# Kernel tuning notes

Hardware: AMD Instinct MI355X
Metric: run time of the kernel (lower is better)

Reference implementation:

```python
import jax, jax.numpy as jnp
import numpy as np

B, S, H, I, E, K = 2, 512, 768, 3072, 8, 1
LB_COEF = 0.01


def _xavier(key, shape, fan_in, fan_out):
    limit = np.sqrt(6.0 / (fan_in + fan_out)).astype(np.float32)
    return jax.random.uniform(key, shape, jnp.float32, -limit, limit)


def setup_inputs() -> dict:
    key = jax.random.key(0)
    k0, k1, k2, k3 = jax.random.split(key, 4)
    return {
        "hidden_states": jax.random.normal(k0, (B, S, H), jnp.float32),
        "gate_w": _xavier(k1, (E, H), H, E),          # nn.Linear(H, E).weight
        "gate_b": jnp.zeros((E,), jnp.float32),
        "w1": _xavier(k2, (E, I, H), H, I),           # per-expert Linear(H, I).weight
        "b1": jnp.zeros((E, I), jnp.float32),
        "w2": _xavier(k3, (E, H, I), I, H),           # per-expert Linear(I, H).weight
        "b2": jnp.zeros((E, H), jnp.float32),
    }


def reference(hidden_states, gate_w, gate_b, w1, b1, w2, b2):
    b, s, h = hidden_states.shape
    x = hidden_states.reshape(-1, h)                      # [T, H]
    gate_logits = x @ gate_w.T + gate_b                   # [T, E]
    top_vals, top_idx = jax.lax.top_k(gate_logits, K)     # [T, K]
    # softmax over the (single) selected logit in fp32 -> all ones, kept for fidelity
    gate_weights = jax.nn.softmax(top_vals.astype(jnp.float32), axis=-1)  # [T, K]

    # load balancing loss (torch.var is unbiased, ddof=1)
    gate_mean = gate_logits.mean(axis=0)                  # [E]
    gate_var = gate_logits.var(axis=0, ddof=1)            # [E]
    lb_loss = LB_COEF * (gate_var / (gate_mean ** 2 + 1e-8)).mean()

    # dense per-expert FFN (exact math; combine picks the routed expert)
    hmid = jnp.einsum('th,eih->tei', x, w1) + b1          # [T, E, I]
    hmid = jax.nn.gelu(hmid, approximate=False)           # torch nn.GELU (erf)
    y = jnp.einsum('tei,ehi->teh', hmid, w2) + b2         # [T, E, H]

    sel = top_idx[:, 0]                                   # [T]
    y_sel = jnp.take_along_axis(y, sel[:, None, None], axis=1)[:, 0]  # [T, H]
    out = y_sel * gate_weights[:, 0:1]                    # weight == 1.0 for k=1
    return out.reshape(b, s, h), lb_loss
```

## Files before the change

kernel.cpp:

```cpp
#include <hip/hip_runtime.h>
#include <hip/hip_bf16.h>
#include <math.h>

#define Hdim 768
#define Idim 3072
#define Tn   1024
#define En   8
#define LD1  72
#define LD2  136

using v4f     = __attribute__((ext_vector_type(4))) float;
using short8  = __attribute__((ext_vector_type(8))) short;
using short4v = __attribute__((ext_vector_type(4))) short;

__device__ inline unsigned short f2bf(float f) {
    unsigned u = __float_as_uint(f);
    u += 0x7fffu + ((u >> 16) & 1u);
    return (unsigned short)(u >> 16);
}
__device__ inline short4v pack4(float4 v) {
    return short4v{ (short)f2bf(v.x), (short)f2bf(v.y), (short)f2bf(v.z), (short)f2bf(v.w) };
}
__device__ __forceinline__ void gl2lds16(const unsigned short* g, unsigned short* l) {
    __builtin_amdgcn_global_load_lds(
        (const __attribute__((address_space(1))) void*)g,
        (__attribute__((address_space(3))) void*)l, 16, 0, 0);
}

__global__ __launch_bounds__(256) void gate_kernel(
    const float* __restrict__ x, const float* __restrict__ gw, const float* __restrict__ gb,
    float* __restrict__ gsum, float* __restrict__ gsumsq,
    int* __restrict__ count, int* __restrict__ sel)
{
    __shared__ float gws[8 * 772];
    __shared__ float lg[8][8];
    int tid = threadIdx.x;
    long t0 = (long)blockIdx.x * 8;
    for (int i = tid; i < 8 * 768; i += 256) gws[(i / 768) * 772 + (i % 768)] = gw[i];
    __syncthreads();

    int tok = tid >> 5, e = (tid >> 2) & 7, qr = tid & 3;
    const float4* xp = (const float4*)(x + (t0 + tok) * Hdim) + qr * 48;
    const float4* gp = (const float4*)(gws + e * 772) + qr * 48;
    float a0 = 0.f, a1 = 0.f;
#pragma unroll 8
    for (int i = 0; i < 48; i += 2) {
        float4 xa = xp[i], ga = gp[i], xc = xp[i + 1], gc = gp[i + 1];
        a0 += xa.x * ga.x + xa.y * ga.y + xa.z * ga.z + xa.w * ga.w;
        a1 += xc.x * gc.x + xc.y * gc.y + xc.z * gc.z + xc.w * gc.w;
    }
    float acc = a0 + a1;
    acc += __shfl_xor(acc, 1);
    acc += __shfl_xor(acc, 2);
    if (qr == 0) lg[tok][e] = acc + gb[e];
    __syncthreads();

    if (tid < 8) {
        float best = lg[tid][0]; int bi = 0;
        for (int j = 1; j < 8; j++) { float v = lg[tid][j]; if (v > best) { best = v; bi = j; } }
        sel[t0 + tid] = bi;
        atomicAdd(&count[bi], 1);
    } else if (tid < 16) {
        int e2 = tid - 8;
        float s = 0.f, ss = 0.f;
        for (int t2 = 0; t2 < 8; t2++) { float v = lg[t2][e2]; s += v; ss += v * v; }
        atomicAdd(&gsum[e2], s);
        atomicAdd(&gsumsq[e2], ss);
    }
}

__global__ void finalize_kernel(const float* __restrict__ gsum, const float* __restrict__ gsumsq,
                                const int* __restrict__ count,
                                int* __restrict__ offsets, int* __restrict__ cursor,
                                float* __restrict__ out_lb)
{
    if (threadIdx.x == 0) {
        float accr = 0.f;
        for (int e = 0; e < 8; e++) {
            float mean = gsum[e] * (1.0f / 1024.0f);
            float var  = (gsumsq[e] - gsum[e] * mean) * (1.0f / 1023.0f);
            accr += var / (mean * mean + 1e-8f);
        }
        out_lb[0] = 0.01f * accr * 0.125f;
        int off = 0;
        for (int e = 0; e < 8; e++) { offsets[e] = off; cursor[e] = off; off += count[e]; }
    }
}

__global__ __launch_bounds__(256) void scatter_kernel(const int* __restrict__ sel,
                                                      int* __restrict__ cursor,
                                                      int* __restrict__ perm)
{
    int t = blockIdx.x * 256 + threadIdx.x;
    if (t < Tn) {
        int e = sel[t];
        int pos = atomicAdd(&cursor[e], 1);
        perm[pos] = t;
    }
}

__global__ __launch_bounds__(256) void gather_x_kernel(const float* __restrict__ x,
                                                       const int* __restrict__ perm,
                                                       unsigned short* __restrict__ xb)
{
    int slot = blockIdx.x * 4 + (threadIdx.x >> 6);
    int lane = threadIdx.x & 63;
    int t = perm[slot];
    const float4* src = (const float4*)(x + (long)t * Hdim);
    unsigned short* dst = xb + (long)slot * Hdim;
#pragma unroll
    for (int i = 0; i < 3; i++) {
        int c = lane + 64 * i;
        *(short4v*)(dst + c * 4) = pack4(src[c]);
    }
}

__global__ __launch_bounds__(256) void init_out_kernel(const float* __restrict__ b2,
                                                       const int* __restrict__ sel,
                                                       float* __restrict__ out)
{
    int t = blockIdx.x;
    int h = blockIdx.y * 256 + threadIdx.x;
    out[(long)t * Hdim + h] = b2[sel[t] * Hdim + h];
}

__global__ __launch_bounds__(256) void gemm1_kernel(
    const unsigned short* __restrict__ xb, const float* __restrict__ w1, const float* __restrict__ b1,
    const int* __restrict__ count, const int* __restrict__ offsets,
    unsigned short* __restrict__ hmid)
{
    int e = blockIdx.z;
    int nloc = count[e];
    int m0 = blockIdx.y << 7;
    if (m0 >= nloc) return;
    int n0 = blockIdx.x << 5;
    int off = offsets[e];

    __shared__ __align__(16) unsigned short As[128 * 64];
    __shared__ __align__(16) unsigned short Bs[32 * LD1];

    int tid = threadIdx.x;
    int lane = tid & 63, wave = tid >> 6;
    int quad = lane >> 4, l16 = lane & 15;
    int wm = wave << 5;

    const unsigned short* aG[4];
    unsigned short* aL[4];
#pragma unroll
    for (int i = 0; i < 4; i++) {
        int p = (wave * 4 + i) * 64 + lane;
        int row = p >> 3;
        int kc = (p & 7) ^ (row & 7);
        int m = m0 + row; int mm = m < nloc ? m : nloc - 1;
        aG[i] = xb + (long)(off + mm) * Hdim + kc * 8;
        aL[i] = (unsigned short*)As + p * 8;
    }
    int kq = tid & 15, rb = tid >> 4;
    const float* bp0 = w1 + ((long)e * Idim + n0 + rb) * Hdim + kq * 4;
    const float* bp1 = bp0 + (long)16 * Hdim;

    v4f acc[2][2];
#pragma unroll
    for (int i = 0; i < 2; i++)
#pragma unroll
        for (int j = 0; j < 2; j++) acc[i][j] = (v4f){0.f, 0.f, 0.f, 0.f};

    float4 nb0 = *(const float4*)bp0;
    float4 nb1 = *(const float4*)bp1;

    for (int kb = 0; kb < Hdim; kb += 64) {
        __syncthreads();
#pragma unroll
        for (int i = 0; i < 4; i++) gl2lds16(aG[i] + kb, aL[i]);
        *(short4v*)(Bs + rb * LD1 + kq * 4)        = pack4(nb0);
        *(short4v*)(Bs + (rb + 16) * LD1 + kq * 4) = pack4(nb1);
        __syncthreads();
        if (kb + 64 < Hdim) {
            nb0 = *(const float4*)(bp0 + kb + 64);
            nb1 = *(const float4*)(bp1 + kb + 64);
        }
#pragma unroll
        for (int s = 0; s < 2; s++) {
            short8 af[2], bf2[2];
#pragma unroll
            for (int i = 0; i < 2; i++) {
                int r = wm + i * 16 + l16;
                af[i] = *(const short8*)(As + r * 64 + (((s * 4 + quad) ^ (r & 7)) * 8));
            }
#pragma unroll
            for (int j = 0; j < 2; j++)
                bf2[j] = *(const short8*)(Bs + (j * 16 + l16) * LD1 + s * 32 + quad * 8);
#pragma unroll
            for (int i = 0; i < 2; i++)
#pragma unroll
                for (int j = 0; j < 2; j++)
                    acc[i][j] = __builtin_amdgcn_mfma_f32_16x16x32_bf16(af[i], bf2[j], acc[i][j], 0, 0, 0);
        }
    }

#pragma unroll
    for (int i = 0; i < 2; i++) {
        int mr = wm + i * 16 + quad * 4;
#pragma unroll
        for (int r = 0; r < 4; r++) {
            int m = m0 + mr + r;
            if (m >= nloc) continue;
            long slot = off + m;
#pragma unroll
            for (int j = 0; j < 2; j++) {
                int n = n0 + j * 16 + l16;
                float v = acc[i][j][r] + b1[e * Idim + n];
                float g = 0.5f * v * (1.0f + erff(v * 0.70710678118654752f));
                hmid[slot * Idim + n] = f2bf(g);
            }
        }
    }
}

__global__ __launch_bounds__(256) void gemm2_kernel(
    const unsigned short* __restrict__ hmid, const float* __restrict__ w2,
    const int* __restrict__ count, const int* __restrict__ offsets,
    const int* __restrict__ perm, float* __restrict__ out)
{
    int e = blockIdx.z;
    int nloc = count[e];
    int m0 = blockIdx.y << 7;
    if (m0 >= nloc) return;
    int bx = blockIdx.x;
    int n0 = (bx % 24) << 5;
    long kbase = (long)(bx / 24) * 768;
    int off = offsets[e];

    __shared__ __align__(16) unsigned short As[128 * 128];
    __shared__ __align__(16) unsigned short Bs[32 * LD2];

    int tid = threadIdx.x;
    int lane = tid & 63, wave = tid >> 6;
    int quad = lane >> 4, l16 = lane & 15;
    int wm = wave << 5;

    const unsigned short* aG[8];
    unsigned short* aL[8];
#pragma unroll
    for (int i = 0; i < 8; i++) {
        int p = (wave * 8 + i) * 64 + lane;
        int row = p >> 4;
        int kc = (p & 15) ^ (row & 15);
        int m = m0 + row; int mm = m < nloc ? m : nloc - 1;
        aG[i] = hmid + (long)(off + mm) * Idim + kbase + kc * 8;
        aL[i] = (unsigned short*)As + p * 8;
    }
    int kq5 = tid & 31, rb8 = tid >> 5;
    const float* bp[4];
#pragma unroll
    for (int s = 0; s < 4; s++)
        bp[s] = w2 + ((long)e * Hdim + n0 + rb8 + 8 * s) * Idim + kbase + kq5 * 4;

    v4f acc[2][2];
#pragma unroll
    for (int i = 0; i < 2; i++)
#pragma unroll
        for (int j = 0; j < 2; j++) acc[i][j] = (v4f){0.f, 0.f, 0.f, 0.f};

    float4 nb[4];
#pragma unroll
    for (int s = 0; s < 4; s++) nb[s] = *(const float4*)bp[s];

    for (int kb = 0; kb < 768; kb += 128) {
        __syncthreads();
#pragma unroll
        for (int i = 0; i < 8; i++) gl2lds16(aG[i] + kb, aL[i]);
#pragma unroll
        for (int s = 0; s < 4; s++)
            *(short4v*)(Bs + (rb8 + 8 * s) * LD2 + kq5 * 4) = pack4(nb[s]);
        __syncthreads();
        if (kb + 128 < 768) {
#pragma unroll
            for (int s = 0; s < 4; s++) nb[s] = *(const float4*)(bp[s] + kb + 128);
        }
#pragma unroll
        for (int s = 0; s < 4; s++) {
            short8 af[2], bf2[2];
#pragma unroll
            for (int i = 0; i < 2; i++) {
                int r = wm + i * 16 + l16;
                af[i] = *(const short8*)(As + r * 128 + (((s * 4 + quad) ^ (r & 15)) * 8));
            }
#pragma unroll
            for (int j = 0; j < 2; j++)
                bf2[j] = *(const short8*)(Bs + (j * 16 + l16) * LD2 + s * 32 + quad * 8);
#pragma unroll
            for (int i = 0; i < 2; i++)
#pragma unroll
                for (int j = 0; j < 2; j++)
                    acc[i][j] = __builtin_amdgcn_mfma_f32_16x16x32_bf16(af[i], bf2[j], acc[i][j], 0, 0, 0);
        }
    }

#pragma unroll
    for (int i = 0; i < 2; i++) {
        int mr = wm + i * 16 + quad * 4;
#pragma unroll
        for (int r = 0; r < 4; r++) {
            int m = m0 + mr + r;
            if (m >= nloc) continue;
            int t = perm[off + m];
#pragma unroll
            for (int j = 0; j < 2; j++) {
                int n = n0 + j * 16 + l16;
                atomicAdd(out + (long)t * Hdim + n, acc[i][j][r]);
            }
        }
    }
}

extern "C" void kernel_launch(void* const* d_in, const int* in_sizes, int n_in,
                              void* d_out, int out_size, void* d_ws, size_t ws_size,
                              hipStream_t stream)
{
    const float* x  = (const float*)d_in[0];
    const float* gw = (const float*)d_in[1];
    const float* gb = (const float*)d_in[2];
    const float* w1 = (const float*)d_in[3];
    const float* b1 = (const float*)d_in[4];
    const float* w2 = (const float*)d_in[5];
    const float* b2 = (const float*)d_in[6];
    float* out = (float*)d_out;

    float* gsum    = (float*)d_ws;
    float* gsumsq  = gsum + 8;
    int*   count   = (int*)d_ws + 16;
    int*   offsets = (int*)d_ws + 24;
    int*   cursor  = (int*)d_ws + 32;
    int*   sel     = (int*)d_ws + 40;
    int*   perm    = (int*)d_ws + 40 + 1024;
    unsigned short* xb   = (unsigned short*)((char*)d_ws + 8704);
    unsigned short* hmid = (unsigned short*)((char*)d_ws + 8704 + (size_t)Tn * Hdim * 2);

    hipMemsetAsync(d_ws, 0, 160, stream);
    gate_kernel<<<128, 256, 0, stream>>>(x, gw, gb, gsum, gsumsq, count, sel);
    finalize_kernel<<<1, 64, 0, stream>>>(gsum, gsumsq, count, offsets, cursor, out + (long)Tn * Hdim);
    scatter_kernel<<<4, 256, 0, stream>>>(sel, cursor, perm);
    gather_x_kernel<<<256, 256, 0, stream>>>(x, perm, xb);
    init_out_kernel<<<dim3(Tn, 3), 256, 0, stream>>>(b2, sel, out);
    gemm1_kernel<<<dim3(96, 2, 8), 256, 0, stream>>>(xb, w1, b1, count, offsets, hmid);
    gemm2_kernel<<<dim3(96, 2, 8), 256, 0, stream>>>(hmid, w2, count, offsets, perm, out);
}
```

Baseline: 240.5 us.

## Enlarge GEMM tiles, fuse finalize+scatter, fold bias into split-K gemm2

Both expert GEMMs move from a 128x32 to a 128x64 output tile with a 2x2 wave layout and K-step 128. Gemm2's split-K changes from 4 slices of 768 to 8 slices of 384. The grid is reordered so that expert index is blockIdx.x, and adjacent blocks work on different experts. Finalize and scatter are merged into one 1024-thread block that uses an LDS cursor. The init_out kernel is replaced by a memset, with b2 added by the first K-slice during the atomic accumulation. The aim is to cut launches and reuse each A tile across more columns, at the cost of more registers, more atomics, and a perm order that is no longer deterministic.

Result: slower. 250.2 us (+4.0%).

```diff
diff --git a/kernel.cpp b/kernel.cpp
--- a/kernel.cpp
+++ b/kernel.cpp
@@ -6,8 +6,7 @@
 #define Idim 3072
 #define Tn   1024
 #define En   8
-#define LD1  72
-#define LD2  136
+#define LDB  136
 
 using v4f     = __attribute__((ext_vector_type(4))) float;
 using short8  = __attribute__((ext_vector_type(8))) short;
@@ -69,12 +68,15 @@
     }
 }
 
-__global__ void finalize_kernel(const float* __restrict__ gsum, const float* __restrict__ gsumsq,
-                                const int* __restrict__ count,
-                                int* __restrict__ offsets, int* __restrict__ cursor,
-                                float* __restrict__ out_lb)
-{
-    if (threadIdx.x == 0) {
+__global__ __launch_bounds__(1024) void finscat_kernel(
+    const float* __restrict__ gsum, const float* __restrict__ gsumsq,
+    const int* __restrict__ count, int* __restrict__ offsets,
+    const int* __restrict__ sel, int* __restrict__ perm,
+    float* __restrict__ out_lb)
+{
+    __shared__ int lcur[8];
+    int tid = threadIdx.x;
+    if (tid == 0) {
         float accr = 0.f;
         for (int e = 0; e < 8; e++) {
             float mean = gsum[e] * (1.0f / 1024.0f);
@@ -83,20 +85,12 @@
         }
         out_lb[0] = 0.01f * accr * 0.125f;
         int off = 0;
-        for (int e = 0; e < 8; e++) { offsets[e] = off; cursor[e] = off; off += count[e]; }
-    }
-}
-
-__global__ __launch_bounds__(256) void scatter_kernel(const int* __restrict__ sel,
-                                                      int* __restrict__ cursor,
-                                                      int* __restrict__ perm)
-{
-    int t = blockIdx.x * 256 + threadIdx.x;
-    if (t < Tn) {
-        int e = sel[t];
-        int pos = atomicAdd(&cursor[e], 1);
-        perm[pos] = t;
-    }
+        for (int e = 0; e < 8; e++) { offsets[e] = off; lcur[e] = off; off += count[e]; }
+    }
+    __syncthreads();
+    int e = sel[tid];
+    int pos = atomicAdd(&lcur[e], 1);
+    perm[pos] = tid;
 }
 
 __global__ __launch_bounds__(256) void gather_x_kernel(const float* __restrict__ x,
@@ -115,83 +109,78 @@
     }
 }
 
-__global__ __launch_bounds__(256) void init_out_kernel(const float* __restrict__ b2,
-                                                       const int* __restrict__ sel,
-                                                       float* __restrict__ out)
-{
-    int t = blockIdx.x;
-    int h = blockIdx.y * 256 + threadIdx.x;
-    out[(long)t * Hdim + h] = b2[sel[t] * Hdim + h];
-}
-
 __global__ __launch_bounds__(256) void gemm1_kernel(
     const unsigned short* __restrict__ xb, const float* __restrict__ w1, const float* __restrict__ b1,
     const int* __restrict__ count, const int* __restrict__ offsets,
     unsigned short* __restrict__ hmid)
 {
-    int e = blockIdx.z;
+    int e = blockIdx.x;
     int nloc = count[e];
-    int m0 = blockIdx.y << 7;
+    int m0 = blockIdx.z << 7;
     if (m0 >= nloc) return;
-    int n0 = blockIdx.x << 5;
+    int n0 = blockIdx.y << 6;
     int off = offsets[e];
 
-    __shared__ __align__(16) unsigned short As[128 * 64];
-    __shared__ __align__(16) unsigned short Bs[32 * LD1];
+    __shared__ __align__(16) unsigned short As[128 * 128];
+    __shared__ __align__(16) unsigned short Bs[64 * LDB];
 
     int tid = threadIdx.x;
     int lane = tid & 63, wave = tid >> 6;
     int quad = lane >> 4, l16 = lane & 15;
-    int wm = wave << 5;
-
-    const unsigned short* aG[4];
-    unsigned short* aL[4];
-#pragma unroll
-    for (int i = 0; i < 4; i++) {
-        int p = (wave * 4 + i) * 64 + lane;
-        int row = p >> 3;
-        int kc = (p & 7) ^ (row & 7);
+    int wm = (wave >> 1) << 6, wn = (wave & 1) << 5;
+
+    const unsigned short* aG[8];
+    unsigned short* aL[8];
+#pragma unroll
+    for (int i = 0; i < 8; i++) {
+        int p = (wave * 8 + i) * 64 + lane;
+        int row = p >> 4;
+        int kc = (p & 15) ^ (row & 15);
         int m = m0 + row; int mm = m < nloc ? m : nloc - 1;
         aG[i] = xb + (long)(off + mm) * Hdim + kc * 8;
         aL[i] = (unsigned short*)As + p * 8;
     }
-    int kq = tid & 15, rb = tid >> 4;
-    const float* bp0 = w1 + ((long)e * Idim + n0 + rb) * Hdim + kq * 4;
-    const float* bp1 = bp0 + (long)16 * Hdim;
-
-    v4f acc[2][2];
-#pragma unroll
-    for (int i = 0; i < 2; i++)
+    int kq5 = tid & 31, rb8 = tid >> 5;
+    const float* bp[8];
+#pragma unroll
+    for (int s = 0; s < 8; s++)
+        bp[s] = w1 + ((long)e * Idim + n0 + rb8 + 8 * s) * Hdim + kq5 * 4;
+
+    v4f acc[4][2];
+#pragma unroll
+    for (int i = 0; i < 4; i++)
 #pragma unroll
         for (int j = 0; j < 2; j++) acc[i][j] = (v4f){0.f, 0.f, 0.f, 0.f};
 
-    float4 nb0 = *(const float4*)bp0;
-    float4 nb1 = *(const float4*)bp1;
-
-    for (int kb = 0; kb < Hdim; kb += 64) {
+    float4 nb[8];
+#pragma unroll
+    for (int s = 0; s < 8; s++) nb[s] = *(const float4*)bp[s];
+
+    for (int kb = 0; kb < Hdim; kb += 128) {
         __syncthreads();
 #pragma unroll
-        for (int i = 0; i < 4; i++) gl2lds16(aG[i] + kb, aL[i]);
-        *(short4v*)(Bs + rb * LD1 + kq * 4)        = pack4(nb0);
-        *(short4v*)(Bs + (rb + 16) * LD1 + kq * 4) = pack4(nb1);
+        for (int i = 0; i < 8; i++) gl2lds16(aG[i] + kb, aL[i]);
+#pragma unroll
+        for (int s = 0; s < 8; s++)
+            *(short4v*)(Bs + (rb8 + 8 * s) * LDB + kq5 * 4) = pack4(nb[s]);
         __syncthreads();
-        if (kb + 64 < Hdim) {
-            nb0 = *(const float4*)(bp0 + kb + 64);
-            nb1 = *(const float4*)(bp1 + kb + 64);
-        }
-#pragma unroll
-        for (int s = 0; s < 2; s++) {
-            short8 af[2], bf2[2];
-#pragma unroll
-            for (int i = 0; i < 2; i++) {
+        if (kb + 128 < Hdim) {
+#pragma unroll
+            for (int s = 0; s < 8; s++) nb[s] = *(const float4*)(bp[s] + kb + 128);
+        }
+#pragma unroll
+        for (int s4 = 0; s4 < 4; s4++) {
+            short8 af[4], bf2[2];
+#pragma unroll
+            for (int i = 0; i < 4; i++) {
                 int r = wm + i * 16 + l16;
-                af[i] = *(const short8*)(As + r * 64 + (((s * 4 + quad) ^ (r & 7)) * 8));
+                af[i] = *(const short8*)(As + r * 128 + (((s4 * 4 + quad) ^ (r & 15)) * 8));
             }
 #pragma unroll
             for (int j = 0; j < 2; j++)
-                bf2[j] = *(const short8*)(Bs + (j * 16 + l16) * LD1 + s * 32 + quad * 8);
-#pragma unroll
-            for (int i = 0; i < 2; i++)
+                bf2[j] = *(const short8*)(Bs + (wn + j * 16 + l16) * LDB + s4 * 32 + quad * 8);
+#pragma unroll
+            for (int i = 0; i < 4; i++)
 #pragma unroll
                 for (int j = 0; j < 2; j++)
                     acc[i][j] = __builtin_amdgcn_mfma_f32_16x16x32_bf16(af[i], bf2[j], acc[i][j], 0, 0, 0);
@@ -199,7 +188,7 @@
     }
 
 #pragma unroll
-    for (int i = 0; i < 2; i++) {
+    for (int i = 0; i < 4; i++) {
         int mr = wm + i * 16 + quad * 4;
 #pragma unroll
         for (int r = 0; r < 4; r++) {
@@ -208,7 +197,7 @@
             long slot = off + m;
 #pragma unroll
             for (int j = 0; j < 2; j++) {
-                int n = n0 + j * 16 + l16;
+                int n = n0 + wn + j * 16 + l16;
                 float v = acc[i][j][r] + b1[e * Idim + n];
                 float g = 0.5f * v * (1.0f + erff(v * 0.70710678118654752f));
                 hmid[slot * Idim + n] = f2bf(g);
@@ -219,25 +208,27 @@
 
 __global__ __launch_bounds__(256) void gemm2_kernel(
     const unsigned short* __restrict__ hmid, const float* __restrict__ w2,
+    const float* __restrict__ b2,
     const int* __restrict__ count, const int* __restrict__ offsets,
     const int* __restrict__ perm, float* __restrict__ out)
 {
-    int e = blockIdx.z;
+    int e = blockIdx.x;
     int nloc = count[e];
-    int m0 = blockIdx.y << 7;
+    int m0 = blockIdx.z << 7;
     if (m0 >= nloc) return;
-    int bx = blockIdx.x;
-    int n0 = (bx % 24) << 5;
-    long kbase = (long)(bx / 24) * 768;
+    int y = blockIdx.y;
+    int sc = y & 7;
+    int n0 = (y >> 3) << 6;
+    long kbase = (long)sc * 384;
     int off = offsets[e];
 
     __shared__ __align__(16) unsigned short As[128 * 128];
-    __shared__ __align__(16) unsigned short Bs[32 * LD2];
+    __shared__ __align__(16) unsigned short Bs[64 * LDB];
 
     int tid = threadIdx.x;
     int lane = tid & 63, wave = tid >> 6;
     int quad = lane >> 4, l16 = lane & 15;
-    int wm = wave << 5;
+    int wm = (wave >> 1) << 6, wn = (wave & 1) << 5;
 
     const unsigned short* aG[8];
     unsigned short* aL[8];
@@ -251,46 +242,46 @@
         aL[i] = (unsigned short*)As + p * 8;
     }
     int kq5 = tid & 31, rb8 = tid >> 5;
-    const float* bp[4];
-#pragma unroll
-    for (int s = 0; s < 4; s++)
+    const float* bp[8];
+#pragma unroll
+    for (int s = 0; s < 8; s++)
         bp[s] = w2 + ((long)e * Hdim + n0 + rb8 + 8 * s) * Idim + kbase + kq5 * 4;
 
-    v4f acc[2][2];
-#pragma unroll
-    for (int i = 0; i < 2; i++)
+    v4f acc[4][2];
+#pragma unroll
+    for (int i = 0; i < 4; i++)
 #pragma unroll
         for (int j = 0; j < 2; j++) acc[i][j] = (v4f){0.f, 0.f, 0.f, 0.f};
 
-    float4 nb[4];
-#pragma unroll
-    for (int s = 0; s < 4; s++) nb[s] = *(const float4*)bp[s];
-
-    for (int kb = 0; kb < 768; kb += 128) {
+    float4 nb[8];
+#pragma unroll
+    for (int s = 0; s < 8; s++) nb[s] = *(const float4*)bp[s];
+
+    for (int kb = 0; kb < 384; kb += 128) {
         __syncthreads();
 #pragma unroll
         for (int i = 0; i < 8; i++) gl2lds16(aG[i] + kb, aL[i]);
 #pragma unroll
-        for (int s = 0; s < 4; s++)
-            *(short4v*)(Bs + (rb8 + 8 * s) * LD2 + kq5 * 4) = pack4(nb[s]);
+        for (int s = 0; s < 8; s++)
+            *(short4v*)(Bs + (rb8 + 8 * s) * LDB + kq5 * 4) = pack4(nb[s]);
         __syncthreads();
-        if (kb + 128 < 768) {
-#pragma unroll
-            for (int s = 0; s < 4; s++) nb[s] = *(const float4*)(bp[s] + kb + 128);
-        }
-#pragma unroll
-        for (int s = 0; s < 4; s++) {
-            short8 af[2], bf2[2];
-#pragma unroll
-            for (int i = 0; i < 2; i++) {
+        if (kb + 128 < 384) {
+#pragma unroll
+            for (int s = 0; s < 8; s++) nb[s] = *(const float4*)(bp[s] + kb + 128);
+        }
+#pragma unroll
+        for (int s4 = 0; s4 < 4; s4++) {
+            short8 af[4], bf2[2];
+#pragma unroll
+            for (int i = 0; i < 4; i++) {
                 int r = wm + i * 16 + l16;
-                af[i] = *(const short8*)(As + r * 128 + (((s * 4 + quad) ^ (r & 15)) * 8));
+                af[i] = *(const short8*)(As + r * 128 + (((s4 * 4 + quad) ^ (r & 15)) * 8));
             }
 #pragma unroll
             for (int j = 0; j < 2; j++)
-                bf2[j] = *(const short8*)(Bs + (j * 16 + l16) * LD2 + s * 32 + quad * 8);
-#pragma unroll
-            for (int i = 0; i < 2; i++)
+                bf2[j] = *(const short8*)(Bs + (wn + j * 16 + l16) * LDB + s4 * 32 + quad * 8);
+#pragma unroll
+            for (int i = 0; i < 4; i++)
 #pragma unroll
                 for (int j = 0; j < 2; j++)
                     acc[i][j] = __builtin_amdgcn_mfma_f32_16x16x32_bf16(af[i], bf2[j], acc[i][j], 0, 0, 0);
@@ -298,7 +289,7 @@
     }
 
 #pragma unroll
-    for (int i = 0; i < 2; i++) {
+    for (int i = 0; i < 4; i++) {
         int mr = wm + i * 16 + quad * 4;
 #pragma unroll
         for (int r = 0; r < 4; r++) {
@@ -307,8 +298,10 @@
             int t = perm[off + m];
 #pragma unroll
             for (int j = 0; j < 2; j++) {
-                int n = n0 + j * 16 + l16;
-                atomicAdd(out + (long)t * Hdim + n, acc[i][j][r]);
+                int n = n0 + wn + j * 16 + l16;
+                float v = acc[i][j][r];
+                if (sc == 0) v += b2[e * Hdim + n];
+                atomicAdd(out + (long)t * Hdim + n, v);
             }
         }
     }
@@ -331,18 +324,17 @@
     float* gsumsq  = gsum + 8;
     int*   count   = (int*)d_ws + 16;
     int*   offsets = (int*)d_ws + 24;
-    int*   cursor  = (int*)d_ws + 32;
     int*   sel     = (int*)d_ws + 40;
     int*   perm    = (int*)d_ws + 40 + 1024;
     unsigned short* xb   = (unsigned short*)((char*)d_ws + 8704);
     unsigned short* hmid = (unsigned short*)((char*)d_ws + 8704 + (size_t)Tn * Hdim * 2);
 
     hipMemsetAsync(d_ws, 0, 160, stream);
+    hipMemsetAsync(out, 0, (size_t)Tn * Hdim * sizeof(float), stream);
     gate_kernel<<<128, 256, 0, stream>>>(x, gw, gb, gsum, gsumsq, count, sel);
-    finalize_kernel<<<1, 64, 0, stream>>>(gsum, gsumsq, count, offsets, cursor, out + (long)Tn * Hdim);
-    scatter_kernel<<<4, 256, 0, stream>>>(sel, cursor, perm);
+    finscat_kernel<<<1, 1024, 0, stream>>>(gsum, gsumsq, count, offsets, sel, perm,
+                                           out + (long)Tn * Hdim);
     gather_x_kernel<<<256, 256, 0, stream>>>(x, perm, xb);
-    init_out_kernel<<<dim3(Tn, 3), 256, 0, stream>>>(b2, sel, out);
-    gemm1_kernel<<<dim3(96, 2, 8), 256, 0, stream>>>(xb, w1, b1, count, offsets, hmid);
-    gemm2_kernel<<<dim3(96, 2, 8), 256, 0, stream>>>(hmid, w2, count, offsets, perm, out);
-}
+    gemm1_kernel<<<dim3(8, 48, 2), 256, 0, stream>>>(xb, w1, b1, count, offsets, hmid);
+    gemm2_kernel<<<dim3(8, 96, 2), 256, 0, stream>>>(hmid, w2, b2, count, offsets, perm, out);
+}
```
